# Kernel optimization log

Measured on AMD Instinct MI355X. Metric: run time of the kernel, lower is better.

The kernel has to match this reference:

```python
import jax, jax.numpy as jnp
import numpy as np

D_MODEL = 1024
NUM_HEADS = 16
D_K = D_MODEL // NUM_HEADS
B, S = 4, 2048
NEG = -1e10


def setup_inputs() -> dict:
    key = jax.random.key(0)
    ks = jax.random.split(key, 12)
    sc = 1.0 / np.sqrt(D_MODEL)
    inp = {
        "q": jax.random.normal(ks[0], (B, S, D_MODEL), jnp.float32),
        "k": jax.random.normal(ks[1], (B, S, D_MODEL), jnp.float32),
        "v": jax.random.normal(ks[2], (B, S, D_MODEL), jnp.float32),
        "mask": jnp.broadcast_to(jnp.tril(jnp.ones((S, S), jnp.int32)), (B, 1, S, S)),
        "w_q": jax.random.normal(ks[3], (D_MODEL, D_MODEL), jnp.float32) * sc,
        "b_q": jax.random.normal(ks[4], (D_MODEL,), jnp.float32) * 0.02,
        "w_k": jax.random.normal(ks[5], (D_MODEL, D_MODEL), jnp.float32) * sc,
        "b_k": jax.random.normal(ks[6], (D_MODEL,), jnp.float32) * 0.02,
        "w_v": jax.random.normal(ks[7], (D_MODEL, D_MODEL), jnp.float32) * sc,
        "b_v": jax.random.normal(ks[8], (D_MODEL,), jnp.float32) * 0.02,
        "w_o": jax.random.normal(ks[9], (D_MODEL, D_MODEL), jnp.float32) * sc,
        "b_o": jax.random.normal(ks[10], (D_MODEL,), jnp.float32) * 0.02,
    }
    return inp


def reference(q, k, v, mask, w_q, b_q, w_k, b_k, w_v, b_v, w_o, b_o):
    b = q.shape[0]
    split = lambda x: x.reshape(b, -1, NUM_HEADS, D_K).transpose(0, 2, 1, 3)  # [B,H,S,d_k]
    Q = split(q @ w_q.T + b_q)
    K = split(k @ w_k.T + b_k)
    V = split(v @ w_v.T + b_v)
    energy = jnp.einsum("bhqd,bhkd->bhqk", Q, K) / jnp.sqrt(jnp.float32(D_K))
    energy = jnp.where(mask == 0, jnp.float32(NEG), energy)
    attn = jax.nn.softmax(energy, axis=-1)
    out = jnp.einsum("bhqk,bhkd->bhqd", attn, V)
    out = out.transpose(0, 2, 1, 3).reshape(b, -1, D_MODEL)
    return out @ w_o.T + b_o
```

## Files before the change

### kernel.cpp

```cpp
#include <hip/hip_runtime.h>

typedef unsigned short u16;
typedef unsigned int u32;
typedef short short8 __attribute__((ext_vector_type(8)));
typedef u16 u16x8 __attribute__((ext_vector_type(8)));
typedef u16 u16x4 __attribute__((ext_vector_type(4)));
typedef float f32x4 __attribute__((ext_vector_type(4)));
typedef float f32x16 __attribute__((ext_vector_type(16)));

__device__ __forceinline__ u16 f2bf(float f) {
  u32 u = __builtin_bit_cast(u32, f);
  u += 0x7fff + ((u >> 16) & 1);
  return (u16)(u >> 16);
}
__device__ __forceinline__ float ex2(float x) {
  float r; asm("v_exp_f32 %0, %1" : "=v"(r) : "v"(x)); return r;
}
__device__ __forceinline__ u32 cvtpk(float lo, float hi) {
  u32 r; asm("v_cvt_pk_bf16_f32 %0, %1, %2" : "=v"(r) : "v"(lo), "v"(hi)); return r;
}

__device__ __forceinline__ void gload16(const u16* g, u16* l) {
  __builtin_amdgcn_global_load_lds(
      (const __attribute__((address_space(1))) u32*)(unsigned long long)(const void*)g,
      (__attribute__((address_space(3))) u32*)(u32)(unsigned long long)(void*)l,
      16, 0, 0);
}

__global__ __launch_bounds__(256) void cvt3(const float* __restrict__ a, const float* __restrict__ b,
                                            const float* __restrict__ c, u16* __restrict__ oa,
                                            u16* __restrict__ ob, u16* __restrict__ oc, int n4) {
  const int z = blockIdx.y;
  const float* s = z == 0 ? a : (z == 1 ? b : c);
  u16* d = z == 0 ? oa : (z == 1 ? ob : oc);
  int i = blockIdx.x * 256 + threadIdx.x;
  if (i >= n4) return;
  float4 f = reinterpret_cast<const float4*>(s)[i];
  u16x4 o;
  o.x = f2bf(f.x); o.y = f2bf(f.y); o.z = f2bf(f.z); o.w = f2bf(f.w);
  reinterpret_cast<u16x4*>(d)[i] = o;
}

__global__ __launch_bounds__(256) void cvt4(const float* __restrict__ a, const float* __restrict__ b,
                                            const float* __restrict__ c, const float* __restrict__ d0,
                                            u16* __restrict__ oa, u16* __restrict__ ob,
                                            u16* __restrict__ oc, u16* __restrict__ od, int n4) {
  const int z = blockIdx.y;
  const float* s = z == 0 ? a : (z == 1 ? b : (z == 2 ? c : d0));
  u16* d = z == 0 ? oa : (z == 1 ? ob : (z == 2 ? oc : od));
  int i = blockIdx.x * 256 + threadIdx.x;
  if (i >= n4) return;
  float4 f = reinterpret_cast<const float4*>(s)[i];
  u16x4 o;
  o.x = f2bf(f.x); o.y = f2bf(f.y); o.z = f2bf(f.z); o.w = f2bf(f.w);
  reinterpret_cast<u16x4*>(d)[i] = o;
}

__device__ __forceinline__ void gemm_core(const u16* __restrict__ A, const u16* __restrict__ Bm,
                                          const float* __restrict__ bias, u16* __restrict__ Cb,
                                          float* __restrict__ Cf, int K, int ldc, int ccol0,
                                          float cs) {
  __shared__ __align__(16) u16 As[2][128 * 32];
  __shared__ __align__(16) u16 Bs[2][128 * 32];
  const int t = threadIdx.x, l = t & 63, w = t >> 6;
  const int lg = l >> 4, lr = l & 15;
  const int m0 = blockIdx.y * 128, n0 = blockIdx.x * 128;
  const int wr = (w >> 1) * 64, wc = (w & 1) * 64;
  const int srow = w * 32 + (l >> 2);
  const int scol = ((l & 3) ^ ((l >> 2) & 3)) * 8;
  const u16* ga = A + (size_t)(m0 + srow) * K + scol;
  const u16* gb = Bm + (size_t)(n0 + srow) * K + scol;
  const int ldst = w * 1024 + l * 8;
  const int ko = (lg ^ (lr & 3)) * 8;

  f32x4 acc[4][4];
#pragma unroll
  for (int i = 0; i < 4; ++i)
#pragma unroll
    for (int jj = 0; jj < 4; ++jj) acc[i][jj] = (f32x4){0.f, 0.f, 0.f, 0.f};

  gload16(ga, &As[0][ldst]);
  gload16(ga + 16 * (size_t)K, &As[0][ldst + 512]);
  gload16(gb, &Bs[0][ldst]);
  gload16(gb + 16 * (size_t)K, &Bs[0][ldst + 512]);
  __syncthreads();

  const int ni = K >> 5;
  for (int it = 0; it < ni; ++it) {
    const int cur = it & 1;
    if (it + 1 < ni) {
      const int k1 = (it + 1) << 5;
      gload16(ga + k1, &As[cur ^ 1][ldst]);
      gload16(ga + k1 + 16 * (size_t)K, &As[cur ^ 1][ldst + 512]);
      gload16(gb + k1, &Bs[cur ^ 1][ldst]);
      gload16(gb + k1 + 16 * (size_t)K, &Bs[cur ^ 1][ldst + 512]);
    }
    short8 af[4], bf[4];
#pragma unroll
    for (int i = 0; i < 4; ++i)
      af[i] = *reinterpret_cast<const short8*>(&As[cur][(wr + 16 * i + lr) * 32 + ko]);
#pragma unroll
    for (int jj = 0; jj < 4; ++jj)
      bf[jj] = *reinterpret_cast<const short8*>(&Bs[cur][(wc + 16 * jj + lr) * 32 + ko]);
#pragma unroll
    for (int i = 0; i < 4; ++i)
#pragma unroll
      for (int jj = 0; jj < 4; ++jj)
        acc[i][jj] = __builtin_amdgcn_mfma_f32_16x16x32_bf16(af[i], bf[jj], acc[i][jj], 0, 0, 0);
    __syncthreads();
  }

#pragma unroll
  for (int i = 0; i < 4; ++i) {
#pragma unroll
    for (int jj = 0; jj < 4; ++jj) {
      int col = n0 + wc + 16 * jj + lr;
      float bv = bias[col];
#pragma unroll
      for (int r = 0; r < 4; ++r) {
        int row = m0 + wr + 16 * i + lg * 4 + r;
        float val = (acc[i][jj][r] + bv) * cs;
        if (Cb) Cb[(size_t)row * ldc + ccol0 + col] = f2bf(val);
        else    Cf[(size_t)row * ldc + col] = val;
      }
    }
  }
}

#define QSCALE 0.18033688011112042f

__global__ __launch_bounds__(256) void gemm_qkv(const u16* __restrict__ Xq, const u16* __restrict__ Xk,
                                                const u16* __restrict__ Xv, const u16* __restrict__ Wq,
                                                const u16* __restrict__ Wk, const u16* __restrict__ Wv,
                                                const float* __restrict__ bq, const float* __restrict__ bk,
                                                const float* __restrict__ bv, u16* __restrict__ QKV) {
  const int z = blockIdx.z;
  const u16* A = z == 0 ? Xq : (z == 1 ? Xk : Xv);
  const u16* B = z == 0 ? Wq : (z == 1 ? Wk : Wv);
  const float* bias = z == 0 ? bq : (z == 1 ? bk : bv);
  gemm_core(A, B, bias, QKV, nullptr, 1024, 3072, z * 1024, z == 0 ? QSCALE : 1.0f);
}

__global__ __launch_bounds__(256) void gemm_out(const u16* __restrict__ AO, const u16* __restrict__ Wo,
                                                const float* __restrict__ bo, float* __restrict__ out) {
  gemm_core(AO, Wo, bo, nullptr, out, 1024, 1024, 0, 1.0f);
}

#define LDK 72
#define DEFER_THR 11.0f

__global__ __launch_bounds__(128, 4) void attn_fwd(const u16* __restrict__ QKV, u16* __restrict__ O) {
  __shared__ __align__(16) u16 Kt[64 * LDK];
  __shared__ __align__(16) u16 Vt[64 * LDK];

  const int t = threadIdx.x, l = t & 63, w = t >> 6;
  const int lq = l & 31, hi = l >> 5;
  const int bh = blockIdx.x;
  const int qb = 31 - (int)blockIdx.y;
  const int b = bh >> 4, h = bh & 15;
  const size_t rowb = (size_t)b * 2048;
  const int qcol = h * 64, kcol = 1024 + h * 64, vcol = 2048 + h * 64;
  const int q0w = qb * 64 + 32 * w;
  const int nt = qb + 1;

  short8 qf[4];
  {
    const u16* qp = QKV + (rowb + q0w + lq) * 3072 + qcol + hi * 8;
#pragma unroll
    for (int ks = 0; ks < 4; ++ks) qf[ks] = *reinterpret_cast<const short8*>(qp + ks * 16);
  }

  f32x16 oa[2];
#pragma unroll
  for (int dt = 0; dt < 2; ++dt)
#pragma unroll
    for (int r = 0; r < 16; ++r) oa[dt][r] = 0.f;
  float m_run = -1e30f, l_run = 0.f;

  const int kr = t & 31;
  const int kc = (t >> 5) * 8;
  const int vr = (t >> 3) * 2;
  const int vc = (t & 7) * 8;
  short8 ka[4];
  u16x8 vv[4];

  auto stage_load = [&](int kv64) {
    const u16* kp = QKV + (rowb + (size_t)kv64 * 64 + kr) * 3072 + kcol + kc;
    ka[0] = *reinterpret_cast<const short8*>(kp);
    ka[1] = *reinterpret_cast<const short8*>(kp + 32);
    ka[2] = *reinterpret_cast<const short8*>(kp + 32 * 3072);
    ka[3] = *reinterpret_cast<const short8*>(kp + 32 * 3072 + 32);
    const u16* vp = QKV + (rowb + (size_t)kv64 * 64 + vr) * 3072 + vcol + vc;
    vv[0] = *reinterpret_cast<const u16x8*>(vp);
    vv[1] = *reinterpret_cast<const u16x8*>(vp + 3072);
    vv[2] = *reinterpret_cast<const u16x8*>(vp + 32 * 3072);
    vv[3] = *reinterpret_cast<const u16x8*>(vp + 33 * 3072);
  };
  auto stage_write = [&]() {
    *reinterpret_cast<short8*>(&Kt[kr * LDK + kc]) = ka[0];
    *reinterpret_cast<short8*>(&Kt[kr * LDK + kc + 32]) = ka[1];
    *reinterpret_cast<short8*>(&Kt[(kr + 32) * LDK + kc]) = ka[2];
    *reinterpret_cast<short8*>(&Kt[(kr + 32) * LDK + kc + 32]) = ka[3];
#pragma unroll
    for (int jj = 0; jj < 8; ++jj) {
      u32 p0 = (u32)vv[0][jj] | ((u32)vv[1][jj] << 16);
      u32 p1 = (u32)vv[2][jj] | ((u32)vv[3][jj] << 16);
      *reinterpret_cast<u32*>(&Vt[(vc + jj) * LDK + vr]) = p0;
      *reinterpret_cast<u32*>(&Vt[(vc + jj) * LDK + vr + 32]) = p1;
    }
  };

  auto flash = [&](int kv0) {
    short8 kf[4], vf[4];
    const int kt32 = (kv0 & 63);
#pragma unroll
    for (int ks = 0; ks < 4; ++ks)
      kf[ks] = *reinterpret_cast<const short8*>(&Kt[(kt32 + lq) * LDK + ks * 16 + hi * 8]);
#pragma unroll
    for (int dt = 0; dt < 2; ++dt)
#pragma unroll
      for (int ks2 = 0; ks2 < 2; ++ks2)
        vf[2 * dt + ks2] = *reinterpret_cast<const short8*>(
            &Vt[(dt * 32 + lq) * LDK + kt32 + ks2 * 16 + hi * 8]);
    f32x16 s;
#pragma unroll
    for (int r = 0; r < 16; ++r) s[r] = 0.f;
    __builtin_amdgcn_s_setprio(1);
#pragma unroll
    for (int ks = 0; ks < 4; ++ks)
      s = __builtin_amdgcn_mfma_f32_32x32x16_bf16(kf[ks], qf[ks], s, 0, 0, 0);
    __builtin_amdgcn_s_setprio(0);
    const bool diag = (kv0 == q0w);
    float p[16];
#pragma unroll
    for (int r = 0; r < 16; ++r) {
      float x = s[r];
      if (diag) {
        int off = (r & 3) + 8 * (r >> 2) + 4 * hi;
        if (off > lq) x = -1e30f;
      }
      p[r] = x;
    }
    float pm = fmaxf(fmaxf(fmaxf(p[0], p[1]), fmaxf(p[2], p[3])),
                     fmaxf(fmaxf(p[4], p[5]), fmaxf(p[6], p[7])));
    pm = fmaxf(pm, fmaxf(fmaxf(fmaxf(p[8], p[9]), fmaxf(p[10], p[11])),
                         fmaxf(fmaxf(p[12], p[13]), fmaxf(p[14], p[15]))));
    pm = fmaxf(pm, __shfl_xor(pm, 32));
    if (!__all(pm <= m_run + DEFER_THR)) {
      float mnew = fmaxf(m_run, pm);
      float al = ex2(m_run - mnew);
      l_run *= al;
#pragma unroll
      for (int dt = 0; dt < 2; ++dt)
#pragma unroll
        for (int r = 0; r < 16; ++r) oa[dt][r] *= al;
      m_run = mnew;
    }
    float ps = 0.f;
#pragma unroll
    for (int r = 0; r < 16; ++r) {
      float e = ex2(p[r] - m_run);
      p[r] = e;
      ps += e;
    }
    ps += __shfl_xor(ps, 32);
    l_run += ps;
    u32 P[8], X[8];
#pragma unroll
    for (int m2 = 0; m2 < 8; ++m2) {
      P[m2] = cvtpk(p[2 * m2], p[2 * m2 + 1]);
      X[m2] = (u32)__shfl_xor((int)P[m2], 32);
    }
    short8 pf[2];
#pragma unroll
    for (int ks2 = 0; ks2 < 2; ++ks2) {
      union { u32 u[4]; short8 v; } uu;
      uu.u[0] = hi ? X[4 * ks2 + 2] : P[4 * ks2 + 0];
      uu.u[1] = hi ? X[4 * ks2 + 3] : P[4 * ks2 + 1];
      uu.u[2] = hi ? P[4 * ks2 + 2] : X[4 * ks2 + 0];
      uu.u[3] = hi ? P[4 * ks2 + 3] : X[4 * ks2 + 1];
      pf[ks2] = uu.v;
    }
    __builtin_amdgcn_s_setprio(1);
#pragma unroll
    for (int ks2 = 0; ks2 < 2; ++ks2)
#pragma unroll
      for (int dt = 0; dt < 2; ++dt)
        oa[dt] = __builtin_amdgcn_mfma_f32_32x32x16_bf16(vf[2 * dt + ks2], pf[ks2], oa[dt], 0, 0, 0);
    __builtin_amdgcn_s_setprio(0);
  };

  stage_load(0);
  stage_write();
  __syncthreads();

  for (int kb = 0; kb < nt; ++kb) {
    if (kb + 1 < nt) stage_load(kb + 1);
#pragma unroll
    for (int kt = 0; kt < 2; ++kt) {
      const int kv0 = kb * 64 + kt * 32;
      if (kv0 <= q0w) flash(kv0);
    }
    __syncthreads();
    if (kb + 1 < nt) stage_write();
    __syncthreads();
  }

  const float inv = __builtin_amdgcn_rcpf(l_run);
  const size_t obase = (rowb + q0w + lq) * 1024 + h * 64;
#pragma unroll
  for (int dt = 0; dt < 2; ++dt) {
    u32 Bp[8], Xb[8];
#pragma unroll
    for (int m2 = 0; m2 < 8; ++m2) {
      Bp[m2] = cvtpk(oa[dt][2 * m2] * inv, oa[dt][2 * m2 + 1] * inv);
      Xb[m2] = (u32)__shfl_xor((int)Bp[m2], 32);
    }
    if (hi == dt) {
#pragma unroll
      for (int c = 0; c < 4; ++c) {
        union { u32 u[4]; short8 v; } uu;
        uu.u[0] = hi ? Xb[2 * c]     : Bp[2 * c];
        uu.u[1] = hi ? Xb[2 * c + 1] : Bp[2 * c + 1];
        uu.u[2] = hi ? Bp[2 * c]     : Xb[2 * c];
        uu.u[3] = hi ? Bp[2 * c + 1] : Xb[2 * c + 1];
        *reinterpret_cast<short8*>(&O[obase + dt * 32 + c * 8]) = uu.v;
      }
    }
  }
}

extern "C" void kernel_launch(void* const* d_in, const int* in_sizes, int n_in,
                              void* d_out, int out_size, void* d_ws, size_t ws_size,
                              hipStream_t stream) {
  const float* q  = (const float*)d_in[0];
  const float* k  = (const float*)d_in[1];
  const float* v  = (const float*)d_in[2];
  const float* wq = (const float*)d_in[4];
  const float* bq = (const float*)d_in[5];
  const float* wk = (const float*)d_in[6];
  const float* bk = (const float*)d_in[7];
  const float* wv = (const float*)d_in[8];
  const float* bv = (const float*)d_in[9];
  const float* wo = (const float*)d_in[10];
  const float* bo = (const float*)d_in[11];
  float* out = (float*)d_out;

  u16* ws = (u16*)d_ws;
  const size_t NE = 8192ull * 1024;
  const size_t WE = 1024ull * 1024;
  u16* Xq   = ws;
  u16* Xk   = Xq + NE;
  u16* Xv   = Xk + NE;
  u16* Wq   = Xv + NE;
  u16* Wk   = Wq + WE;
  u16* Wv   = Wk + WE;
  u16* Wo   = Wv + WE;
  u16* QKVp = Wo + WE;
  u16* AO   = QKVp + 8192ull * 3072;

  cvt3<<<dim3(8192, 3), 256, 0, stream>>>(q, k, v, Xq, Xk, Xv, (int)(NE / 4));
  cvt4<<<dim3(1024, 4), 256, 0, stream>>>(wq, wk, wv, wo, Wq, Wk, Wv, Wo, (int)(WE / 4));

  gemm_qkv<<<dim3(8, 64, 3), 256, 0, stream>>>(Xq, Xk, Xv, Wq, Wk, Wv, bq, bk, bv, QKVp);

  attn_fwd<<<dim3(64, 32), 128, 0, stream>>>(QKVp, AO);

  gemm_out<<<dim3(8, 64), 256, 0, stream>>>(AO, Wo, bo, out);
}
```

Measured before the change: 409.9 us.

## Triple-buffer GEMM loads and enlarge attention blocks to 128 query rows

The GEMM core moves from double to triple buffering of its LDS tiles. It uses explicit vmcnt waits and raw barriers instead of __syncthreads, raises wave priority around the MFMA block, and changes the LDS swizzle pattern. Separately, the attention kernel now uses 256 threads per block covering 128 query rows, so each staged K/V tile is shared by four waves, and the per-thread staging work is halved. The aim is to hide global-load latency in the GEMMs and cut redundant K/V loads in attention, at the cost of more LDS per GEMM block and coarser causal work granularity.

```diff
diff --git a/kernel.cpp b/kernel.cpp
--- a/kernel.cpp
+++ b/kernel.cpp
@@ -60,18 +60,21 @@
                                           const float* __restrict__ bias, u16* __restrict__ Cb,
                                           float* __restrict__ Cf, int K, int ldc, int ccol0,
                                           float cs) {
-  __shared__ __align__(16) u16 As[2][128 * 32];
-  __shared__ __align__(16) u16 Bs[2][128 * 32];
+  __shared__ __align__(16) u16 As[3][128 * 32];
+  __shared__ __align__(16) u16 Bs[3][128 * 32];
   const int t = threadIdx.x, l = t & 63, w = t >> 6;
   const int lg = l >> 4, lr = l & 15;
   const int m0 = blockIdx.y * 128, n0 = blockIdx.x * 128;
   const int wr = (w >> 1) * 64, wc = (w & 1) * 64;
   const int srow = w * 32 + (l >> 2);
-  const int scol = ((l & 3) ^ ((l >> 2) & 3)) * 8;
+  const int scol = ((l & 3) ^ ((l >> 3) & 3)) * 8;
   const u16* ga = A + (size_t)(m0 + srow) * K + scol;
   const u16* gb = Bm + (size_t)(n0 + srow) * K + scol;
   const int ldst = w * 1024 + l * 8;
-  const int ko = (lg ^ (lr & 3)) * 8;
+  const int ko = (lg ^ ((lr >> 1) & 3)) * 8;
+
+  u16* a0 = &As[0][0]; u16* a1 = &As[1][0]; u16* a2 = &As[2][0];
+  u16* b0 = &Bs[0][0]; u16* b1 = &Bs[1][0]; u16* b2 = &Bs[2][0];
 
   f32x4 acc[4][4];
 #pragma unroll
@@ -79,35 +82,51 @@
 #pragma unroll
     for (int jj = 0; jj < 4; ++jj) acc[i][jj] = (f32x4){0.f, 0.f, 0.f, 0.f};
 
-  gload16(ga, &As[0][ldst]);
-  gload16(ga + 16 * (size_t)K, &As[0][ldst + 512]);
-  gload16(gb, &Bs[0][ldst]);
-  gload16(gb + 16 * (size_t)K, &Bs[0][ldst + 512]);
-  __syncthreads();
-
   const int ni = K >> 5;
+  gload16(ga, a0 + ldst);
+  gload16(ga + 16 * (size_t)K, a0 + ldst + 512);
+  gload16(gb, b0 + ldst);
+  gload16(gb + 16 * (size_t)K, b0 + ldst + 512);
+  gload16(ga + 32, a1 + ldst);
+  gload16(ga + 32 + 16 * (size_t)K, a1 + ldst + 512);
+  gload16(gb + 32, b1 + ldst);
+  gload16(gb + 32 + 16 * (size_t)K, b1 + ldst + 512);
+  asm volatile("s_waitcnt vmcnt(4)" ::: "memory");
+  __builtin_amdgcn_s_barrier();
+  __builtin_amdgcn_sched_barrier(0);
+
   for (int it = 0; it < ni; ++it) {
-    const int cur = it & 1;
-    if (it + 1 < ni) {
-      const int k1 = (it + 1) << 5;
-      gload16(ga + k1, &As[cur ^ 1][ldst]);
-      gload16(ga + k1 + 16 * (size_t)K, &As[cur ^ 1][ldst + 512]);
-      gload16(gb + k1, &Bs[cur ^ 1][ldst]);
-      gload16(gb + k1 + 16 * (size_t)K, &Bs[cur ^ 1][ldst + 512]);
+    const bool pf = (it + 2) < ni;
+    if (pf) {
+      const int k2 = (it + 2) << 5;
+      gload16(ga + k2, a2 + ldst);
+      gload16(ga + k2 + 16 * (size_t)K, a2 + ldst + 512);
+      gload16(gb + k2, b2 + ldst);
+      gload16(gb + k2 + 16 * (size_t)K, b2 + ldst + 512);
     }
     short8 af[4], bf[4];
 #pragma unroll
     for (int i = 0; i < 4; ++i)
-      af[i] = *reinterpret_cast<const short8*>(&As[cur][(wr + 16 * i + lr) * 32 + ko]);
+      af[i] = *reinterpret_cast<const short8*>(&a0[(wr + 16 * i + lr) * 32 + ko]);
 #pragma unroll
     for (int jj = 0; jj < 4; ++jj)
-      bf[jj] = *reinterpret_cast<const short8*>(&Bs[cur][(wc + 16 * jj + lr) * 32 + ko]);
+      bf[jj] = *reinterpret_cast<const short8*>(&b0[(wc + 16 * jj + lr) * 32 + ko]);
+    __builtin_amdgcn_s_setprio(1);
 #pragma unroll
     for (int i = 0; i < 4; ++i)
 #pragma unroll
       for (int jj = 0; jj < 4; ++jj)
         acc[i][jj] = __builtin_amdgcn_mfma_f32_16x16x32_bf16(af[i], bf[jj], acc[i][jj], 0, 0, 0);
-    __syncthreads();
+    __builtin_amdgcn_s_setprio(0);
+    if (it + 1 < ni) {
+      if (pf) asm volatile("s_waitcnt vmcnt(4)" ::: "memory");
+      else    asm volatile("s_waitcnt vmcnt(0)" ::: "memory");
+      __builtin_amdgcn_s_barrier();
+      __builtin_amdgcn_sched_barrier(0);
+    }
+    u16* tmp;
+    tmp = a0; a0 = a1; a1 = a2; a2 = tmp;
+    tmp = b0; b0 = b1; b1 = b2; b2 = tmp;
   }
 
 #pragma unroll
@@ -149,19 +168,19 @@
 #define LDK 72
 #define DEFER_THR 11.0f
 
-__global__ __launch_bounds__(128, 4) void attn_fwd(const u16* __restrict__ QKV, u16* __restrict__ O) {
+__global__ __launch_bounds__(256, 4) void attn_fwd(const u16* __restrict__ QKV, u16* __restrict__ O) {
   __shared__ __align__(16) u16 Kt[64 * LDK];
   __shared__ __align__(16) u16 Vt[64 * LDK];
 
   const int t = threadIdx.x, l = t & 63, w = t >> 6;
   const int lq = l & 31, hi = l >> 5;
   const int bh = blockIdx.x;
-  const int qb = 31 - (int)blockIdx.y;
+  const int qb = 15 - (int)blockIdx.y;
   const int b = bh >> 4, h = bh & 15;
   const size_t rowb = (size_t)b * 2048;
   const int qcol = h * 64, kcol = 1024 + h * 64, vcol = 2048 + h * 64;
-  const int q0w = qb * 64 + 32 * w;
-  const int nt = qb + 1;
+  const int q0w = qb * 128 + 32 * w;
+  const int nt = 2 * qb + 2;
 
   short8 qf[4];
   {
@@ -177,36 +196,25 @@
     for (int r = 0; r < 16; ++r) oa[dt][r] = 0.f;
   float m_run = -1e30f, l_run = 0.f;
 
-  const int kr = t & 31;
-  const int kc = (t >> 5) * 8;
-  const int vr = (t >> 3) * 2;
-  const int vc = (t & 7) * 8;
-  short8 ka[4];
-  u16x8 vv[4];
+  const int kr = t & 31, kc = (t >> 5) * 8;
+  short8 ka0, ka1;
+  u16x8 va0, va1;
 
   auto stage_load = [&](int kv64) {
     const u16* kp = QKV + (rowb + (size_t)kv64 * 64 + kr) * 3072 + kcol + kc;
-    ka[0] = *reinterpret_cast<const short8*>(kp);
-    ka[1] = *reinterpret_cast<const short8*>(kp + 32);
-    ka[2] = *reinterpret_cast<const short8*>(kp + 32 * 3072);
-    ka[3] = *reinterpret_cast<const short8*>(kp + 32 * 3072 + 32);
-    const u16* vp = QKV + (rowb + (size_t)kv64 * 64 + vr) * 3072 + vcol + vc;
-    vv[0] = *reinterpret_cast<const u16x8*>(vp);
-    vv[1] = *reinterpret_cast<const u16x8*>(vp + 3072);
-    vv[2] = *reinterpret_cast<const u16x8*>(vp + 32 * 3072);
-    vv[3] = *reinterpret_cast<const u16x8*>(vp + 33 * 3072);
+    ka0 = *reinterpret_cast<const short8*>(kp);
+    ka1 = *reinterpret_cast<const short8*>(kp + 32 * 3072);
+    const u16* vp = QKV + (rowb + (size_t)kv64 * 64 + 2 * kr) * 3072 + vcol + kc;
+    va0 = *reinterpret_cast<const u16x8*>(vp);
+    va1 = *reinterpret_cast<const u16x8*>(vp + 3072);
   };
   auto stage_write = [&]() {
-    *reinterpret_cast<short8*>(&Kt[kr * LDK + kc]) = ka[0];
-    *reinterpret_cast<short8*>(&Kt[kr * LDK + kc + 32]) = ka[1];
-    *reinterpret_cast<short8*>(&Kt[(kr + 32) * LDK + kc]) = ka[2];
-    *reinterpret_cast<short8*>(&Kt[(kr + 32) * LDK + kc + 32]) = ka[3];
+    *reinterpret_cast<short8*>(&Kt[kr * LDK + kc]) = ka0;
+    *reinterpret_cast<short8*>(&Kt[(kr + 32) * LDK + kc]) = ka1;
 #pragma unroll
     for (int jj = 0; jj < 8; ++jj) {
-      u32 p0 = (u32)vv[0][jj] | ((u32)vv[1][jj] << 16);
-      u32 p1 = (u32)vv[2][jj] | ((u32)vv[3][jj] << 16);
-      *reinterpret_cast<u32*>(&Vt[(vc + jj) * LDK + vr]) = p0;
-      *reinterpret_cast<u32*>(&Vt[(vc + jj) * LDK + vr + 32]) = p1;
+      u32 pk = (u32)va0[jj] | ((u32)va1[jj] << 16);
+      *reinterpret_cast<u32*>(&Vt[(kc + jj) * LDK + 2 * kr]) = pk;
     }
   };
 
@@ -364,7 +372,7 @@
 
   gemm_qkv<<<dim3(8, 64, 3), 256, 0, stream>>>(Xq, Xk, Xv, Wq, Wk, Wv, bq, bk, bv, QKVp);
 
-  attn_fwd<<<dim3(64, 32), 128, 0, stream>>>(QKVp, AO);
+  attn_fwd<<<dim3(64, 16), 256, 0, stream>>>(QKVp, AO);
 
   gemm_out<<<dim3(8, 64), 256, 0, stream>>>(AO, Wo, bo, out);
 }
```

Measured after the change: 373.9 us. 8.8% less time.
